# Performance work log

Measured on AMD Instinct MI355X. Metric: run time of the kernel, lower is better.

## Reference

```python
import jax, jax.numpy as jnp
import numpy as np

N_NODES = 10000
N_EDGES = 640000
IN_C = 128
HID = 256
OUT_C = 256


def _linear_params(key, fan_in, fan_out):
    k1, k2 = jax.random.split(key)
    bound = 1.0 / np.sqrt(fan_in)
    W = jax.random.uniform(k1, (fan_in, fan_out), jnp.float32, -bound, bound)
    b = jax.random.uniform(k2, (fan_out,), jnp.float32, -bound, bound)
    return W, b


def setup_inputs() -> dict:
    key = jax.random.key(0)
    ks = jax.random.split(key, 8)
    x = jax.random.normal(ks[0], (N_NODES, IN_C), jnp.float32)
    edge_index = jax.random.randint(ks[1], (2, N_EDGES), 0, N_NODES, jnp.int32)
    W0a, b0a = _linear_params(ks[2], IN_C, HID)
    W0b, b0b = _linear_params(ks[3], HID, HID)
    W1a, b1a = _linear_params(ks[4], HID, HID)
    W1b, b1b = _linear_params(ks[5], HID, HID)
    W2a, b2a = _linear_params(ks[6], HID, OUT_C)
    W2b, b2b = _linear_params(ks[7], OUT_C, OUT_C)
    return {"x": x, "edge_index": edge_index,
            "W0a": W0a, "b0a": b0a, "W0b": W0b, "b0b": b0b,
            "W1a": W1a, "b1a": b1a, "W1b": W1b, "b1b": b1b,
            "W2a": W2a, "b2a": b2a, "W2b": W2b, "b2b": b2b}


def _gin_conv(x, src, dst, Wa, ba, Wb, bb):
    # sum-aggregate neighbor features: agg[i] = sum_{(j->i) in E} x[j]
    agg = jax.ops.segment_sum(x[src], dst, num_segments=N_NODES)
    h = x + agg  # eps = 0 (PyG GINConv default): (1+eps)*x + agg
    h = jnp.maximum(h @ Wa + ba, 0.0) @ Wb + bb  # Linear-ReLU-Linear MLP
    return h


def reference(x, edge_index, W0a, b0a, W0b, b0b, W1a, b1a, W1b, b1b, W2a, b2a, W2b, b2b):
    src, dst = edge_index[0], edge_index[1]
    h = _gin_conv(x, src, dst, W0a, b0a, W0b, b0b)
    h = jnp.maximum(h, 0.0)  # ReLU; dropout is identity in eval mode
    h = _gin_conv(h, src, dst, W1a, b1a, W1b, b1b)
    h = jnp.maximum(h, 0.0)
    h = _gin_conv(h, src, dst, W2a, b2a, W2b, b2b)
    return h
```

## Files before the change

kernel.cpp:

```cpp
#include <hip/hip_runtime.h>

#define N_NODES 10000
#define N_EDGES 640000
#define ELL_W   128
#define NB      157
#define BCAP    4600
#define LCAP    80
#define CHUNK   2500

typedef short short8 __attribute__((ext_vector_type(8)));
typedef float f32x4 __attribute__((ext_vector_type(4)));

__device__ inline float bf2f(unsigned short u) {
    return __uint_as_float(((unsigned)u) << 16);
}
__device__ inline unsigned short f2bf(float f) {
    unsigned u = __float_as_uint(f);
    u += 0x7fffu + ((u >> 16) & 1u);
    return (unsigned short)(u >> 16);
}

__global__ __launch_bounds__(256) void bin_edges(const int* __restrict__ src,
                                                 const int* __restrict__ dst,
                                                 int* __restrict__ gCursor,
                                                 unsigned* __restrict__ gBucket) {
    __shared__ unsigned bins[NB][LCAP];
    __shared__ int cnt[NB];
    __shared__ int base[NB];
    int t = threadIdx.x;
    for (int i = t; i < NB; i += 256) cnt[i] = 0;
    __syncthreads();

    int e0 = blockIdx.x * CHUNK;
    int e1 = min(e0 + CHUNK, N_EDGES);
    for (int e = e0 + t; e < e1; e += 256) {
        int d = dst[e];
        int b = d >> 6;
        unsigned pk = ((unsigned)src[e] << 6) | (unsigned)(d & 63);
        int p = atomicAdd(&cnt[b], 1);
        if (p < LCAP) bins[b][p] = pk;
    }
    __syncthreads();
    for (int i = t; i < NB; i += 256) {
        int c = min(cnt[i], LCAP);
        cnt[i] = c;
        base[i] = atomicAdd(&gCursor[i], c);
    }
    __syncthreads();
    int wave = t >> 6, lane = t & 63;
    for (int b = wave; b < NB; b += 4) {
        int ba = base[b];
        int n = min(cnt[b], max(0, BCAP - ba));
        for (int i = lane; i < n; i += 64)
            gBucket[(size_t)b * BCAP + ba + i] = bins[b][i];
    }
}

__global__ __launch_bounds__(256) void build_ell(const unsigned* __restrict__ gBucket,
                                                 const int* __restrict__ gCursor,
                                                 unsigned short* __restrict__ ell,
                                                 int* __restrict__ deg) {
    __shared__ unsigned short rows[64 * ELL_W];
    __shared__ int ldeg[64];
    int b = blockIdx.x;
    int t = threadIdx.x;
    for (int i = t; i < 64; i += 256) ldeg[i] = 0;
    __syncthreads();

    int n = min(gCursor[b], BCAP);
    const unsigned* bk = gBucket + (size_t)b * BCAP;
    for (int i = t; i < n; i += 256) {
        unsigned pk = bk[i];
        int local = pk & 63;
        int s = pk >> 6;
        int p = atomicAdd(&ldeg[local], 1);
        if (p < ELL_W) rows[local * ELL_W + p] = (unsigned short)s;
    }
    __syncthreads();

    int node0 = b * 64;
    int nNodes = min(64, N_NODES - node0);
    if (nNodes <= 0) return;
    for (int i = t; i < nNodes; i += 256)
        deg[node0 + i] = min(ldeg[i], ELL_W);
    int totalVec = nNodes * (ELL_W / 8);
    short8* dstv = (short8*)(ell + (size_t)node0 * ELL_W);
    const short8* srcv = (const short8*)rows;
    for (int i = t; i < totalVec; i += 256) dstv[i] = srcv[i];
}

struct WList {
    const float* src[6];
    unsigned short* dst[6];
    int K[6];
    int off[7];
};

__global__ __launch_bounds__(256) void prep_kernel(const float4* __restrict__ x,
                                                   ushort4* __restrict__ xb, int n4,
                                                   WList wl, int totalW,
                                                   int* __restrict__ gCursor) {
    int idx = blockIdx.x * 256 + threadIdx.x;
    if (blockIdx.x == 0 && threadIdx.x < NB) gCursor[threadIdx.x] = 0;
    if (idx < n4) {
        float4 v = x[idx];
        ushort4 o;
        o.x = f2bf(v.x); o.y = f2bf(v.y); o.z = f2bf(v.z); o.w = f2bf(v.w);
        xb[idx] = o;
        return;
    }
    int r0 = idx - n4;
    if (r0 >= totalW) return;
    int w = 0;
    while (r0 >= wl.off[w + 1]) ++w;
    int r = r0 - wl.off[w];
    int k = r >> 8;
    int n = r & 255;
    wl.dst[w][(size_t)n * wl.K[w] + k] = f2bf(wl.src[w][r]);
}

template <int U2STRIDE>
__global__ __launch_bounds__(256) void gather_ell(const unsigned* __restrict__ x,
                                                  const unsigned short* __restrict__ ell,
                                                  const int* __restrict__ deg,
                                                  unsigned* __restrict__ out) {
    int wid = (blockIdx.x * 256 + threadIdx.x) >> 6;
    int lane = threadIdx.x & 63;
    if (wid >= N_NODES) return;
    int off = blockIdx.y * 64 + lane;

    unsigned v = x[(size_t)wid * U2STRIDE + off];
    float a0 = bf2f((unsigned short)(v & 0xffff));
    float a1 = bf2f((unsigned short)(v >> 16));

    int dg = min(deg[wid], ELL_W);
    const unsigned short* row = ell + (size_t)wid * ELL_W;

    int j = 0;
    for (; j + 16 <= dg; j += 16) {
        short8 iA = *(const short8*)(row + j);
        short8 iB = *(const short8*)(row + j + 8);
        unsigned vv[16];
#pragma unroll
        for (int q = 0; q < 8; ++q)
            vv[q] = x[(size_t)(unsigned short)iA[q] * U2STRIDE + off];
#pragma unroll
        for (int q = 0; q < 8; ++q)
            vv[8 + q] = x[(size_t)(unsigned short)iB[q] * U2STRIDE + off];
#pragma unroll
        for (int q = 0; q < 16; ++q) {
            a0 += bf2f((unsigned short)(vv[q] & 0xffff));
            a1 += bf2f((unsigned short)(vv[q] >> 16));
        }
    }
    for (; j + 4 <= dg; j += 4) {
        ushort4 sA = *(const ushort4*)(row + j);
        unsigned v0 = x[(size_t)sA.x * U2STRIDE + off];
        unsigned v1 = x[(size_t)sA.y * U2STRIDE + off];
        unsigned v2 = x[(size_t)sA.z * U2STRIDE + off];
        unsigned v3 = x[(size_t)sA.w * U2STRIDE + off];
        a0 += (bf2f((unsigned short)(v0 & 0xffff)) + bf2f((unsigned short)(v1 & 0xffff))) +
              (bf2f((unsigned short)(v2 & 0xffff)) + bf2f((unsigned short)(v3 & 0xffff)));
        a1 += (bf2f((unsigned short)(v0 >> 16)) + bf2f((unsigned short)(v1 >> 16))) +
              (bf2f((unsigned short)(v2 >> 16)) + bf2f((unsigned short)(v3 >> 16)));
    }
    for (; j < dg; ++j) {
        unsigned vv = x[(size_t)row[j] * U2STRIDE + off];
        a0 += bf2f((unsigned short)(vv & 0xffff));
        a1 += bf2f((unsigned short)(vv >> 16));
    }
    unsigned o = (unsigned)f2bf(a0) | ((unsigned)f2bf(a1) << 16);
    out[(size_t)wid * U2STRIDE + off] = o;
}

template <int KSTEPS, bool RELU2, bool F32OUT>
__global__ __launch_bounds__(256) void mlp_mfma(const unsigned short* __restrict__ A,
                                                const unsigned short* __restrict__ WtA,
                                                const float* __restrict__ biasA,
                                                const unsigned short* __restrict__ WtB,
                                                const float* __restrict__ biasB,
                                                void* __restrict__ Cout) {
    constexpr int K1 = KSTEPS * 32;
    constexpr int LP = 264;
    __shared__ unsigned short hid[32 * LP];

    int r0 = blockIdx.x * 32;
    int tid = threadIdx.x;
    int lane = tid & 63;
    int nq = tid >> 6;
    int lrow = lane & 15;
    int lkg = lane >> 4;
    int n0 = nq * 64;

    {
        const short8* Ap0 = (const short8*)(A + (size_t)(r0 + lrow) * K1 + lkg * 8);
        const short8* Ap1 = (const short8*)(A + (size_t)(r0 + 16 + lrow) * K1 + lkg * 8);
        const short8* Bp = (const short8*)(WtA + (size_t)(n0 + lrow) * K1 + lkg * 8);
        f32x4 acc[2][4] = {};
#pragma unroll
        for (int ks = 0; ks < KSTEPS; ++ks) {
            short8 a0 = Ap0[ks * 4];
            short8 a1 = Ap1[ks * 4];
            short8 b0 = Bp[ks * 4 + 0 * 2 * K1];
            short8 b1 = Bp[ks * 4 + 1 * 2 * K1];
            short8 b2 = Bp[ks * 4 + 2 * 2 * K1];
            short8 b3 = Bp[ks * 4 + 3 * 2 * K1];
            acc[0][0] = __builtin_amdgcn_mfma_f32_16x16x32_bf16(a0, b0, acc[0][0], 0, 0, 0);
            acc[0][1] = __builtin_amdgcn_mfma_f32_16x16x32_bf16(a0, b1, acc[0][1], 0, 0, 0);
            acc[0][2] = __builtin_amdgcn_mfma_f32_16x16x32_bf16(a0, b2, acc[0][2], 0, 0, 0);
            acc[0][3] = __builtin_amdgcn_mfma_f32_16x16x32_bf16(a0, b3, acc[0][3], 0, 0, 0);
            acc[1][0] = __builtin_amdgcn_mfma_f32_16x16x32_bf16(a1, b0, acc[1][0], 0, 0, 0);
            acc[1][1] = __builtin_amdgcn_mfma_f32_16x16x32_bf16(a1, b1, acc[1][1], 0, 0, 0);
            acc[1][2] = __builtin_amdgcn_mfma_f32_16x16x32_bf16(a1, b2, acc[1][2], 0, 0, 0);
            acc[1][3] = __builtin_amdgcn_mfma_f32_16x16x32_bf16(a1, b3, acc[1][3], 0, 0, 0);
        }
#pragma unroll
        for (int rg = 0; rg < 2; ++rg) {
            int row = rg * 16 + lkg * 4;
#pragma unroll
            for (int nt = 0; nt < 4; ++nt) {
                int c = n0 + nt * 16 + lrow;
                float bv = biasA[c];
#pragma unroll
                for (int r = 0; r < 4; ++r) {
                    float v = fmaxf(acc[rg][nt][r] + bv, 0.f);
                    hid[(row + r) * LP + c] = f2bf(v);
                }
            }
        }
    }
    __syncthreads();

    {
        const short8* Bp = (const short8*)(WtB + (size_t)(n0 + lrow) * 256 + lkg * 8);
        f32x4 acc[2][4] = {};
#pragma unroll
        for (int ks = 0; ks < 8; ++ks) {
            short8 a0 = *(const short8*)&hid[lrow * LP + ks * 32 + lkg * 8];
            short8 a1 = *(const short8*)&hid[(16 + lrow) * LP + ks * 32 + lkg * 8];
            short8 b0 = Bp[ks * 4 + 0 * 2 * 256];
            short8 b1 = Bp[ks * 4 + 1 * 2 * 256];
            short8 b2 = Bp[ks * 4 + 2 * 2 * 256];
            short8 b3 = Bp[ks * 4 + 3 * 2 * 256];
            acc[0][0] = __builtin_amdgcn_mfma_f32_16x16x32_bf16(a0, b0, acc[0][0], 0, 0, 0);
            acc[0][1] = __builtin_amdgcn_mfma_f32_16x16x32_bf16(a0, b1, acc[0][1], 0, 0, 0);
            acc[0][2] = __builtin_amdgcn_mfma_f32_16x16x32_bf16(a0, b2, acc[0][2], 0, 0, 0);
            acc[0][3] = __builtin_amdgcn_mfma_f32_16x16x32_bf16(a0, b3, acc[0][3], 0, 0, 0);
            acc[1][0] = __builtin_amdgcn_mfma_f32_16x16x32_bf16(a1, b0, acc[1][0], 0, 0, 0);
            acc[1][1] = __builtin_amdgcn_mfma_f32_16x16x32_bf16(a1, b1, acc[1][1], 0, 0, 0);
            acc[1][2] = __builtin_amdgcn_mfma_f32_16x16x32_bf16(a1, b2, acc[1][2], 0, 0, 0);
            acc[1][3] = __builtin_amdgcn_mfma_f32_16x16x32_bf16(a1, b3, acc[1][3], 0, 0, 0);
        }
#pragma unroll
        for (int rg = 0; rg < 2; ++rg) {
            int orow = r0 + rg * 16 + lkg * 4;
#pragma unroll
            for (int nt = 0; nt < 4; ++nt) {
                int c = n0 + nt * 16 + lrow;
                float bv = biasB[c];
#pragma unroll
                for (int r = 0; r < 4; ++r) {
                    int grow = orow + r;
                    if (grow >= N_NODES) continue;
                    float v = acc[rg][nt][r] + bv;
                    if (RELU2) v = fmaxf(v, 0.f);
                    if (F32OUT)
                        ((float*)Cout)[(size_t)grow * 256 + c] = v;
                    else
                        ((unsigned short*)Cout)[(size_t)grow * 256 + c] = f2bf(v);
                }
            }
        }
    }
}

extern "C" void kernel_launch(void* const* d_in, const int* in_sizes, int n_in,
                              void* d_out, int out_size, void* d_ws, size_t ws_size,
                              hipStream_t stream) {
    const float* x   = (const float*)d_in[0];
    const int*   ei  = (const int*)d_in[1];
    const int*   src = ei;
    const int*   dst = ei + N_EDGES;
    const float* W0a = (const float*)d_in[2];
    const float* b0a = (const float*)d_in[3];
    const float* W0b = (const float*)d_in[4];
    const float* b0b = (const float*)d_in[5];
    const float* W1a = (const float*)d_in[6];
    const float* b1a = (const float*)d_in[7];
    const float* W1b = (const float*)d_in[8];
    const float* b1b = (const float*)d_in[9];
    const float* W2a = (const float*)d_in[10];
    const float* b2a = (const float*)d_in[11];
    const float* W2b = (const float*)d_in[12];
    const float* b2b = (const float*)d_in[13];

    char* ws = (char*)d_ws;
    size_t off = 0;
    auto alloc = [&](size_t bytes) {
        void* p = ws + off;
        off += (bytes + 255) & ~(size_t)255;
        return p;
    };
    unsigned short* xb    = (unsigned short*)alloc((size_t)N_NODES * 128 * 2);
    unsigned short* B0    = (unsigned short*)alloc((size_t)N_NODES * 256 * 2);
    unsigned short* B2    = (unsigned short*)alloc((size_t)N_NODES * 256 * 2);
    unsigned short* Wt0a  = (unsigned short*)alloc(256 * 128 * 2);
    unsigned short* Wt0b  = (unsigned short*)alloc(256 * 256 * 2);
    unsigned short* Wt1a  = (unsigned short*)alloc(256 * 256 * 2);
    unsigned short* Wt1b  = (unsigned short*)alloc(256 * 256 * 2);
    unsigned short* Wt2a  = (unsigned short*)alloc(256 * 256 * 2);
    unsigned short* Wt2b  = (unsigned short*)alloc(256 * 256 * 2);
    int*            deg   = (int*)alloc(N_NODES * 4);
    unsigned short* ell   = (unsigned short*)alloc((size_t)N_NODES * ELL_W * 2);
    int*            gCur  = (int*)alloc(NB * 4);
    unsigned*       gBkt  = (unsigned*)alloc((size_t)NB * BCAP * 4);

    dim3 gatherGrid1((N_NODES + 3) / 4, 1);
    dim3 gatherGrid2((N_NODES + 3) / 4, 2);
    int mlpBlocks = (N_NODES + 31) / 32;

    WList wl;
    wl.src[0] = W0a; wl.dst[0] = Wt0a; wl.K[0] = 128;
    wl.src[1] = W0b; wl.dst[1] = Wt0b; wl.K[1] = 256;
    wl.src[2] = W1a; wl.dst[2] = Wt1a; wl.K[2] = 256;
    wl.src[3] = W1b; wl.dst[3] = Wt1b; wl.K[3] = 256;
    wl.src[4] = W2a; wl.dst[4] = Wt2a; wl.K[4] = 256;
    wl.src[5] = W2b; wl.dst[5] = Wt2b; wl.K[5] = 256;
    int totalW = 0;
    for (int i = 0; i < 6; ++i) { wl.off[i] = totalW; totalW += wl.K[i] * 256; }
    wl.off[6] = totalW;
    int n4 = N_NODES * 128 / 4;
    int prepTasks = n4 + totalW;
    prep_kernel<<<(prepTasks + 255) / 256, 256, 0, stream>>>(
        (const float4*)x, (ushort4*)xb, n4, wl, totalW, gCur);

    bin_edges<<<(N_EDGES + CHUNK - 1) / CHUNK, 256, 0, stream>>>(src, dst, gCur, gBkt);
    build_ell<<<NB, 256, 0, stream>>>(gBkt, gCur, ell, deg);

    gather_ell<64><<<gatherGrid1, 256, 0, stream>>>((const unsigned*)xb, ell, deg, (unsigned*)B0);
    mlp_mfma<4, true, false><<<mlpBlocks, 256, 0, stream>>>(B0, Wt0a, b0a, Wt0b, b0b, B2);
    gather_ell<128><<<gatherGrid2, 256, 0, stream>>>((const unsigned*)B2, ell, deg, (unsigned*)B0);
    mlp_mfma<8, true, false><<<mlpBlocks, 256, 0, stream>>>(B0, Wt1a, b1a, Wt1b, b1b, B2);
    gather_ell<128><<<gatherGrid2, 256, 0, stream>>>((const unsigned*)B2, ell, deg, (unsigned*)B0);
    mlp_mfma<8, false, true><<<mlpBlocks, 256, 0, stream>>>(B0, Wt2a, b2a, Wt2b, b2b, d_out);
}
```

Before: 161.1 us.

## Widen gather to uint2 per lane, halve MLP row tile, shrink binning chunks

For 256-wide layers the gather kernel now has each lane load 8 bytes (uint2), so one wave covers a full row instead of splitting it across two grid-y blocks. This reads each row's neighbor index list once instead of twice and gives wider memory transactions. The MLP kernel now processes 16 rows per block instead of 32, doubling the block count for better occupancy but loading the weight tiles more times. Edge-binning chunk size and local bin capacity are also reduced, which increases the number of binning blocks.

```diff
diff --git a/kernel.cpp b/kernel.cpp
--- a/kernel.cpp
+++ b/kernel.cpp
@@ -5,8 +5,8 @@
 #define ELL_W   128
 #define NB      157
 #define BCAP    4600
-#define LCAP    80
-#define CHUNK   2500
+#define LCAP    64
+#define CHUNK   1250
 
 typedef short short8 __attribute__((ext_vector_type(8)));
 typedef float f32x4 __attribute__((ext_vector_type(4)));
@@ -119,58 +119,110 @@
     wl.dst[w][(size_t)n * wl.K[w] + k] = f2bf(wl.src[w][r]);
 }
 
-template <int U2STRIDE>
-__global__ __launch_bounds__(256) void gather_ell(const unsigned* __restrict__ x,
+template <int UPL>
+__global__ __launch_bounds__(256) void gather_ell(const void* __restrict__ xv,
                                                   const unsigned short* __restrict__ ell,
                                                   const int* __restrict__ deg,
-                                                  unsigned* __restrict__ out) {
+                                                  void* __restrict__ outv) {
     int wid = (blockIdx.x * 256 + threadIdx.x) >> 6;
     int lane = threadIdx.x & 63;
     if (wid >= N_NODES) return;
-    int off = blockIdx.y * 64 + lane;
-
-    unsigned v = x[(size_t)wid * U2STRIDE + off];
-    float a0 = bf2f((unsigned short)(v & 0xffff));
-    float a1 = bf2f((unsigned short)(v >> 16));
-
     int dg = min(deg[wid], ELL_W);
     const unsigned short* row = ell + (size_t)wid * ELL_W;
 
-    int j = 0;
-    for (; j + 16 <= dg; j += 16) {
-        short8 iA = *(const short8*)(row + j);
-        short8 iB = *(const short8*)(row + j + 8);
-        unsigned vv[16];
-#pragma unroll
-        for (int q = 0; q < 8; ++q)
-            vv[q] = x[(size_t)(unsigned short)iA[q] * U2STRIDE + off];
-#pragma unroll
-        for (int q = 0; q < 8; ++q)
-            vv[8 + q] = x[(size_t)(unsigned short)iB[q] * U2STRIDE + off];
-#pragma unroll
-        for (int q = 0; q < 16; ++q) {
-            a0 += bf2f((unsigned short)(vv[q] & 0xffff));
-            a1 += bf2f((unsigned short)(vv[q] >> 16));
-        }
-    }
-    for (; j + 4 <= dg; j += 4) {
-        ushort4 sA = *(const ushort4*)(row + j);
-        unsigned v0 = x[(size_t)sA.x * U2STRIDE + off];
-        unsigned v1 = x[(size_t)sA.y * U2STRIDE + off];
-        unsigned v2 = x[(size_t)sA.z * U2STRIDE + off];
-        unsigned v3 = x[(size_t)sA.w * U2STRIDE + off];
-        a0 += (bf2f((unsigned short)(v0 & 0xffff)) + bf2f((unsigned short)(v1 & 0xffff))) +
-              (bf2f((unsigned short)(v2 & 0xffff)) + bf2f((unsigned short)(v3 & 0xffff)));
-        a1 += (bf2f((unsigned short)(v0 >> 16)) + bf2f((unsigned short)(v1 >> 16))) +
-              (bf2f((unsigned short)(v2 >> 16)) + bf2f((unsigned short)(v3 >> 16)));
-    }
-    for (; j < dg; ++j) {
-        unsigned vv = x[(size_t)row[j] * U2STRIDE + off];
-        a0 += bf2f((unsigned short)(vv & 0xffff));
-        a1 += bf2f((unsigned short)(vv >> 16));
-    }
-    unsigned o = (unsigned)f2bf(a0) | ((unsigned)f2bf(a1) << 16);
-    out[(size_t)wid * U2STRIDE + off] = o;
+    if (UPL == 1) {
+        const unsigned* x = (const unsigned*)xv;
+        unsigned v = x[(size_t)wid * 64 + lane];
+        float a0 = bf2f((unsigned short)(v & 0xffff));
+        float a1 = bf2f((unsigned short)(v >> 16));
+        int j = 0;
+        for (; j + 16 <= dg; j += 16) {
+            short8 iA = *(const short8*)(row + j);
+            short8 iB = *(const short8*)(row + j + 8);
+            unsigned vv[16];
+#pragma unroll
+            for (int q = 0; q < 8; ++q)
+                vv[q] = x[(size_t)(unsigned short)iA[q] * 64 + lane];
+#pragma unroll
+            for (int q = 0; q < 8; ++q)
+                vv[8 + q] = x[(size_t)(unsigned short)iB[q] * 64 + lane];
+#pragma unroll
+            for (int q = 0; q < 16; ++q) {
+                a0 += bf2f((unsigned short)(vv[q] & 0xffff));
+                a1 += bf2f((unsigned short)(vv[q] >> 16));
+            }
+        }
+        for (; j + 4 <= dg; j += 4) {
+            ushort4 sA = *(const ushort4*)(row + j);
+            unsigned v0 = x[(size_t)sA.x * 64 + lane];
+            unsigned v1 = x[(size_t)sA.y * 64 + lane];
+            unsigned v2 = x[(size_t)sA.z * 64 + lane];
+            unsigned v3 = x[(size_t)sA.w * 64 + lane];
+            a0 += (bf2f((unsigned short)(v0 & 0xffff)) + bf2f((unsigned short)(v1 & 0xffff))) +
+                  (bf2f((unsigned short)(v2 & 0xffff)) + bf2f((unsigned short)(v3 & 0xffff)));
+            a1 += (bf2f((unsigned short)(v0 >> 16)) + bf2f((unsigned short)(v1 >> 16))) +
+                  (bf2f((unsigned short)(v2 >> 16)) + bf2f((unsigned short)(v3 >> 16)));
+        }
+        for (; j < dg; ++j) {
+            unsigned vv = x[(size_t)row[j] * 64 + lane];
+            a0 += bf2f((unsigned short)(vv & 0xffff));
+            a1 += bf2f((unsigned short)(vv >> 16));
+        }
+        ((unsigned*)outv)[(size_t)wid * 64 + lane] =
+            (unsigned)f2bf(a0) | ((unsigned)f2bf(a1) << 16);
+    } else {
+        const uint2* x = (const uint2*)xv;
+        uint2 v = x[(size_t)wid * 64 + lane];
+        float a0 = bf2f((unsigned short)(v.x & 0xffff));
+        float a1 = bf2f((unsigned short)(v.x >> 16));
+        float a2 = bf2f((unsigned short)(v.y & 0xffff));
+        float a3 = bf2f((unsigned short)(v.y >> 16));
+        int j = 0;
+        for (; j + 16 <= dg; j += 16) {
+            short8 iA = *(const short8*)(row + j);
+            short8 iB = *(const short8*)(row + j + 8);
+            uint2 vv[16];
+#pragma unroll
+            for (int q = 0; q < 8; ++q)
+                vv[q] = x[(size_t)(unsigned short)iA[q] * 64 + lane];
+#pragma unroll
+            for (int q = 0; q < 8; ++q)
+                vv[8 + q] = x[(size_t)(unsigned short)iB[q] * 64 + lane];
+#pragma unroll
+            for (int q = 0; q < 16; ++q) {
+                a0 += bf2f((unsigned short)(vv[q].x & 0xffff));
+                a1 += bf2f((unsigned short)(vv[q].x >> 16));
+                a2 += bf2f((unsigned short)(vv[q].y & 0xffff));
+                a3 += bf2f((unsigned short)(vv[q].y >> 16));
+            }
+        }
+        for (; j + 4 <= dg; j += 4) {
+            ushort4 sA = *(const ushort4*)(row + j);
+            uint2 v0 = x[(size_t)sA.x * 64 + lane];
+            uint2 v1 = x[(size_t)sA.y * 64 + lane];
+            uint2 v2 = x[(size_t)sA.z * 64 + lane];
+            uint2 v3 = x[(size_t)sA.w * 64 + lane];
+            a0 += (bf2f((unsigned short)(v0.x & 0xffff)) + bf2f((unsigned short)(v1.x & 0xffff))) +
+                  (bf2f((unsigned short)(v2.x & 0xffff)) + bf2f((unsigned short)(v3.x & 0xffff)));
+            a1 += (bf2f((unsigned short)(v0.x >> 16)) + bf2f((unsigned short)(v1.x >> 16))) +
+                  (bf2f((unsigned short)(v2.x >> 16)) + bf2f((unsigned short)(v3.x >> 16)));
+            a2 += (bf2f((unsigned short)(v0.y & 0xffff)) + bf2f((unsigned short)(v1.y & 0xffff))) +
+                  (bf2f((unsigned short)(v2.y & 0xffff)) + bf2f((unsigned short)(v3.y & 0xffff)));
+            a3 += (bf2f((unsigned short)(v0.y >> 16)) + bf2f((unsigned short)(v1.y >> 16))) +
+                  (bf2f((unsigned short)(v2.y >> 16)) + bf2f((unsigned short)(v3.y >> 16)));
+        }
+        for (; j < dg; ++j) {
+            uint2 vv = x[(size_t)row[j] * 64 + lane];
+            a0 += bf2f((unsigned short)(vv.x & 0xffff));
+            a1 += bf2f((unsigned short)(vv.x >> 16));
+            a2 += bf2f((unsigned short)(vv.y & 0xffff));
+            a3 += bf2f((unsigned short)(vv.y >> 16));
+        }
+        uint2 o;
+        o.x = (unsigned)f2bf(a0) | ((unsigned)f2bf(a1) << 16);
+        o.y = (unsigned)f2bf(a2) | ((unsigned)f2bf(a3) << 16);
+        ((uint2*)outv)[(size_t)wid * 64 + lane] = o;
+    }
 }
 
 template <int KSTEPS, bool RELU2, bool F32OUT>
@@ -182,9 +234,9 @@
                                                 void* __restrict__ Cout) {
     constexpr int K1 = KSTEPS * 32;
     constexpr int LP = 264;
-    __shared__ unsigned short hid[32 * LP];
-
-    int r0 = blockIdx.x * 32;
+    __shared__ unsigned short hid[16 * LP];
+
+    int r0 = blockIdx.x * 16;
     int tid = threadIdx.x;
     int lane = tid & 63;
     int nq = tid >> 6;
@@ -193,39 +245,30 @@
     int n0 = nq * 64;
 
     {
-        const short8* Ap0 = (const short8*)(A + (size_t)(r0 + lrow) * K1 + lkg * 8);
-        const short8* Ap1 = (const short8*)(A + (size_t)(r0 + 16 + lrow) * K1 + lkg * 8);
+        const short8* Ap = (const short8*)(A + (size_t)(r0 + lrow) * K1 + lkg * 8);
         const short8* Bp = (const short8*)(WtA + (size_t)(n0 + lrow) * K1 + lkg * 8);
-        f32x4 acc[2][4] = {};
+        f32x4 acc[4] = {};
 #pragma unroll
         for (int ks = 0; ks < KSTEPS; ++ks) {
-            short8 a0 = Ap0[ks * 4];
-            short8 a1 = Ap1[ks * 4];
+            short8 a = Ap[ks * 4];
             short8 b0 = Bp[ks * 4 + 0 * 2 * K1];
             short8 b1 = Bp[ks * 4 + 1 * 2 * K1];
             short8 b2 = Bp[ks * 4 + 2 * 2 * K1];
             short8 b3 = Bp[ks * 4 + 3 * 2 * K1];
-            acc[0][0] = __builtin_amdgcn_mfma_f32_16x16x32_bf16(a0, b0, acc[0][0], 0, 0, 0);
-            acc[0][1] = __builtin_amdgcn_mfma_f32_16x16x32_bf16(a0, b1, acc[0][1], 0, 0, 0);
-            acc[0][2] = __builtin_amdgcn_mfma_f32_16x16x32_bf16(a0, b2, acc[0][2], 0, 0, 0);
-            acc[0][3] = __builtin_amdgcn_mfma_f32_16x16x32_bf16(a0, b3, acc[0][3], 0, 0, 0);
-            acc[1][0] = __builtin_amdgcn_mfma_f32_16x16x32_bf16(a1, b0, acc[1][0], 0, 0, 0);
-            acc[1][1] = __builtin_amdgcn_mfma_f32_16x16x32_bf16(a1, b1, acc[1][1], 0, 0, 0);
-            acc[1][2] = __builtin_amdgcn_mfma_f32_16x16x32_bf16(a1, b2, acc[1][2], 0, 0, 0);
-            acc[1][3] = __builtin_amdgcn_mfma_f32_16x16x32_bf16(a1, b3, acc[1][3], 0, 0, 0);
-        }
-#pragma unroll
-        for (int rg = 0; rg < 2; ++rg) {
-            int row = rg * 16 + lkg * 4;
-#pragma unroll
-            for (int nt = 0; nt < 4; ++nt) {
-                int c = n0 + nt * 16 + lrow;
-                float bv = biasA[c];
-#pragma unroll
-                for (int r = 0; r < 4; ++r) {
-                    float v = fmaxf(acc[rg][nt][r] + bv, 0.f);
-                    hid[(row + r) * LP + c] = f2bf(v);
-                }
+            acc[0] = __builtin_amdgcn_mfma_f32_16x16x32_bf16(a, b0, acc[0], 0, 0, 0);
+            acc[1] = __builtin_amdgcn_mfma_f32_16x16x32_bf16(a, b1, acc[1], 0, 0, 0);
+            acc[2] = __builtin_amdgcn_mfma_f32_16x16x32_bf16(a, b2, acc[2], 0, 0, 0);
+            acc[3] = __builtin_amdgcn_mfma_f32_16x16x32_bf16(a, b3, acc[3], 0, 0, 0);
+        }
+        int row = lkg * 4;
+#pragma unroll
+        for (int nt = 0; nt < 4; ++nt) {
+            int c = n0 + nt * 16 + lrow;
+            float bv = biasA[c];
+#pragma unroll
+            for (int r = 0; r < 4; ++r) {
+                float v = fmaxf(acc[nt][r] + bv, 0.f);
+                hid[(row + r) * LP + c] = f2bf(v);
             }
         }
     }
@@ -233,42 +276,34 @@
 
     {
         const short8* Bp = (const short8*)(WtB + (size_t)(n0 + lrow) * 256 + lkg * 8);
-        f32x4 acc[2][4] = {};
+        f32x4 acc[4] = {};
 #pragma unroll
         for (int ks = 0; ks < 8; ++ks) {
-            short8 a0 = *(const short8*)&hid[lrow * LP + ks * 32 + lkg * 8];
-            short8 a1 = *(const short8*)&hid[(16 + lrow) * LP + ks * 32 + lkg * 8];
+            short8 a = *(const short8*)&hid[lrow * LP + ks * 32 + lkg * 8];
             short8 b0 = Bp[ks * 4 + 0 * 2 * 256];
             short8 b1 = Bp[ks * 4 + 1 * 2 * 256];
             short8 b2 = Bp[ks * 4 + 2 * 2 * 256];
             short8 b3 = Bp[ks * 4 + 3 * 2 * 256];
-            acc[0][0] = __builtin_amdgcn_mfma_f32_16x16x32_bf16(a0, b0, acc[0][0], 0, 0, 0);
-            acc[0][1] = __builtin_amdgcn_mfma_f32_16x16x32_bf16(a0, b1, acc[0][1], 0, 0, 0);
-            acc[0][2] = __builtin_amdgcn_mfma_f32_16x16x32_bf16(a0, b2, acc[0][2], 0, 0, 0);
-            acc[0][3] = __builtin_amdgcn_mfma_f32_16x16x32_bf16(a0, b3, acc[0][3], 0, 0, 0);
-            acc[1][0] = __builtin_amdgcn_mfma_f32_16x16x32_bf16(a1, b0, acc[1][0], 0, 0, 0);
-            acc[1][1] = __builtin_amdgcn_mfma_f32_16x16x32_bf16(a1, b1, acc[1][1], 0, 0, 0);
-            acc[1][2] = __builtin_amdgcn_mfma_f32_16x16x32_bf16(a1, b2, acc[1][2], 0, 0, 0);
-            acc[1][3] = __builtin_amdgcn_mfma_f32_16x16x32_bf16(a1, b3, acc[1][3], 0, 0, 0);
-        }
-#pragma unroll
-        for (int rg = 0; rg < 2; ++rg) {
-            int orow = r0 + rg * 16 + lkg * 4;
-#pragma unroll
-            for (int nt = 0; nt < 4; ++nt) {
-                int c = n0 + nt * 16 + lrow;
-                float bv = biasB[c];
-#pragma unroll
-                for (int r = 0; r < 4; ++r) {
-                    int grow = orow + r;
-                    if (grow >= N_NODES) continue;
-                    float v = acc[rg][nt][r] + bv;
-                    if (RELU2) v = fmaxf(v, 0.f);
-                    if (F32OUT)
-                        ((float*)Cout)[(size_t)grow * 256 + c] = v;
-                    else
-                        ((unsigned short*)Cout)[(size_t)grow * 256 + c] = f2bf(v);
-                }
+            acc[0] = __builtin_amdgcn_mfma_f32_16x16x32_bf16(a, b0, acc[0], 0, 0, 0);
+            acc[1] = __builtin_amdgcn_mfma_f32_16x16x32_bf16(a, b1, acc[1], 0, 0, 0);
+            acc[2] = __builtin_amdgcn_mfma_f32_16x16x32_bf16(a, b2, acc[2], 0, 0, 0);
+            acc[3] = __builtin_amdgcn_mfma_f32_16x16x32_bf16(a, b3, acc[3], 0, 0, 0);
+        }
+        int orow = r0 + lkg * 4;
+#pragma unroll
+        for (int nt = 0; nt < 4; ++nt) {
+            int c = n0 + nt * 16 + lrow;
+            float bv = biasB[c];
+#pragma unroll
+            for (int r = 0; r < 4; ++r) {
+                int grow = orow + r;
+                if (grow >= N_NODES) continue;
+                float v = acc[nt][r] + bv;
+                if (RELU2) v = fmaxf(v, 0.f);
+                if (F32OUT)
+                    ((float*)Cout)[(size_t)grow * 256 + c] = v;
+                else
+                    ((unsigned short*)Cout)[(size_t)grow * 256 + c] = f2bf(v);
             }
         }
     }
@@ -315,9 +350,8 @@
     int*            gCur  = (int*)alloc(NB * 4);
     unsigned*       gBkt  = (unsigned*)alloc((size_t)NB * BCAP * 4);
 
-    dim3 gatherGrid1((N_NODES + 3) / 4, 1);
-    dim3 gatherGrid2((N_NODES + 3) / 4, 2);
-    int mlpBlocks = (N_NODES + 31) / 32;
+    int gatherBlocks = (N_NODES + 3) / 4;
+    int mlpBlocks = (N_NODES + 15) / 16;
 
     WList wl;
     wl.src[0] = W0a; wl.dst[0] = Wt0a; wl.K[0] = 128;
@@ -337,10 +371,10 @@
     bin_edges<<<(N_EDGES + CHUNK - 1) / CHUNK, 256, 0, stream>>>(src, dst, gCur, gBkt);
     build_ell<<<NB, 256, 0, stream>>>(gBkt, gCur, ell, deg);
 
-    gather_ell<64><<<gatherGrid1, 256, 0, stream>>>((const unsigned*)xb, ell, deg, (unsigned*)B0);
+    gather_ell<1><<<gatherBlocks, 256, 0, stream>>>(xb, ell, deg, B0);
     mlp_mfma<4, true, false><<<mlpBlocks, 256, 0, stream>>>(B0, Wt0a, b0a, Wt0b, b0b, B2);
-    gather_ell<128><<<gatherGrid2, 256, 0, stream>>>((const unsigned*)B2, ell, deg, (unsigned*)B0);
+    gather_ell<2><<<gatherBlocks, 256, 0, stream>>>(B2, ell, deg, B0);
     mlp_mfma<8, true, false><<<mlpBlocks, 256, 0, stream>>>(B0, Wt1a, b1a, Wt1b, b1b, B2);
-    gather_ell<128><<<gatherGrid2, 256, 0, stream>>>((const unsigned*)B2, ell, deg, (unsigned*)B0);
+    gather_ell<2><<<gatherBlocks, 256, 0, stream>>>(B2, ell, deg, B0);
     mlp_mfma<8, false, true><<<mlpBlocks, 256, 0, stream>>>(B0, Wt2a, b2a, Wt2b, b2b, d_out);
 }
```

Result: slower. 189.6 us (+17.7%).
